# Performance work log

Measured on AMD Instinct MI355X. Metric: run time of the kernel, lower is better.

The kernel has to match this reference:

```python
import jax, jax.numpy as jnp
import numpy as np

EMBED_DIM = 384
MAX_LEN = 5000
TIMESTEP = 10000.0


def _build_table():
    pos = np.arange(MAX_LEN, dtype=np.float32)[:, None]
    div = np.exp(np.arange(0, EMBED_DIM, 2, dtype=np.float32) * (-np.log(TIMESTEP) / EMBED_DIM))
    pe = np.zeros((MAX_LEN, EMBED_DIM), dtype=np.float32)
    pe[:, 0::2] = np.sin(pos * div)
    pe[:, 1::2] = np.cos(pos * div)
    return jnp.asarray(pe)


def setup_inputs() -> dict:
    key = jax.random.key(0)
    x = jax.random.randint(key, (32, 512), 0, 16, dtype=jnp.int32)  # per-token durations
    pos_enc = _build_table()  # (MAX_LEN, EMBED_DIM) learned-free sinusoidal table
    return {"x": x, "pos_enc": pos_enc}


def reference(x, pos_enc):
    # x: (B, N) int durations; output: (B, T, D), T = max row-total frames
    cs = jnp.cumsum(x, axis=1)                 # (B, N) cumulative frame counts
    total = cs[:, -1]                          # (B,) frames per row
    T = int(np.asarray(jnp.max(cs)))           # concrete max total frames (data-dep, eval eagerly)
    starts = cs - x                            # (B, N) start frame of each token
    t = jnp.arange(T, dtype=cs.dtype)          # (T,) frame indices
    # token owning each frame: first index with cs > t
    tok = jax.vmap(lambda c: jnp.searchsorted(c, t, side='right'))(cs)  # (B, T)
    tok = jnp.minimum(tok, x.shape[1] - 1)     # clamp for padded frames
    pos = t[None, :] - jnp.take_along_axis(starts, tok, axis=1)         # (B, T) within-token position
    valid = t[None, :] < total[:, None]        # (B, T)
    pos = jnp.where(valid, pos, 0)
    emb = pos_enc[pos]                         # (B, T, D) gather
    return emb * valid[..., None].astype(emb.dtype)
```

## Files before the change

### kernel.cpp

```cpp
#include <hip/hip_runtime.h>
#include <hip/hip_bf16.h>


#define B 32
#define L 512
#define D 384
#define D4 (D / 4)

__global__ __launch_bounds__(64) void pe_cumsum_kernel(
    const int* __restrict__ x, int* __restrict__ cs) {
  const int b = blockIdx.x;
  const int lane = threadIdx.x;
  const int base = b * L + lane * 8;

  const int4* xr = reinterpret_cast<const int4*>(x + base);
  int4 a = xr[0];
  int4 c = xr[1];
  int v[8] = {a.x, a.y, a.z, a.w, c.x, c.y, c.z, c.w};

  int pref[8];
  int s = 0;
#pragma unroll
  for (int k = 0; k < 8; ++k) { s += v[k]; pref[k] = s; }

  int acc = s;
#pragma unroll
  for (int off = 1; off < 64; off <<= 1) {
    int n = __shfl_up(acc, off);
    if (lane >= off) acc += n;
  }
  const int offset = acc - s;

  int4 o0 = make_int4(offset + pref[0], offset + pref[1],
                      offset + pref[2], offset + pref[3]);
  int4 o1 = make_int4(offset + pref[4], offset + pref[5],
                      offset + pref[6], offset + pref[7]);
  int4* cr = reinterpret_cast<int4*>(cs + base);
  cr[0] = o0;
  cr[1] = o1;
}

__global__ __launch_bounds__(256) void pe_segcopy_kernel(
    const int* __restrict__ x, const int* __restrict__ cs,
    const float4* __restrict__ pe, float4* __restrict__ out, int T) {
  const int j = blockIdx.x;
  const int b = blockIdx.y;
  const int c = x[b * L + j];
  if (c == 0) return;
  const int start = cs[b * L + j] - c;

  float4* dst = out + ((size_t)b * T + start) * D4;
  const int n = c * D4;
  for (int i = threadIdx.x; i < n; i += 256) {
    dst[i] = pe[i];
  }
}

__global__ __launch_bounds__(256) void pe_tailzero_kernel(
    const int* __restrict__ cs, float4* __restrict__ out, int T) {
  const int b = blockIdx.y;
  const int total = cs[b * L + (L - 1)];
  const int n = (T - total) * D4;
  float4* dst = out + ((size_t)b * T + total) * D4;
  const float4 z = make_float4(0.f, 0.f, 0.f, 0.f);
  const int stride = gridDim.x * 256;
  for (int i = blockIdx.x * 256 + threadIdx.x; i < n; i += stride) {
    dst[i] = z;
  }
}

extern "C" void kernel_launch(void* const* d_in, const int* in_sizes, int n_in,
                              void* d_out, int out_size, void* d_ws, size_t ws_size,
                              hipStream_t stream) {
  const int* x = (const int*)d_in[0];
  const float* pe = (const float*)d_in[1];
  float* out = (float*)d_out;

  const int T = out_size / (B * D);

  int* cs = (int*)d_ws;

  pe_cumsum_kernel<<<B, 64, 0, stream>>>(x, cs);

  dim3 g2(L, B);
  pe_segcopy_kernel<<<g2, 256, 0, stream>>>(x, cs, (const float4*)pe,
                                            (float4*)out, T);

  dim3 g3(32, B);
  pe_tailzero_kernel<<<g3, 256, 0, stream>>>(cs, (float4*)out, T);
}
```

Measured before the change: 202.1 us.

## Build per-frame source-row map, then write output in one flat streaming kernel

The plan kernel now writes, for each output frame, the within-token position (or -1 for padding) into a workspace array. One grid-stride kernel then fills the whole output: each element looks up its row's source and copies a pe vector or writes zero, using nontemporal stores. This replaces the per-token segment-copy blocks, many of them tiny or empty, and the separate tail-zero kernel with one evenly balanced launch. The cost is that the plan kernel fills the map serially per lane, and the write kernel does an integer divide and an extra index load per element.

```diff
diff --git a/kernel.cpp b/kernel.cpp
--- a/kernel.cpp
+++ b/kernel.cpp
@@ -7,16 +7,18 @@
 #define D 384
 #define D4 (D / 4)
 
-__global__ __launch_bounds__(64) void pe_cumsum_kernel(
-    const int* __restrict__ x, int* __restrict__ cs) {
+typedef float f32x4 __attribute__((ext_vector_type(4)));
+
+__global__ __launch_bounds__(64) void pe_plan_kernel(
+    const int* __restrict__ x, int* __restrict__ rowsrc, int T) {
   const int b = blockIdx.x;
   const int lane = threadIdx.x;
   const int base = b * L + lane * 8;
 
   const int4* xr = reinterpret_cast<const int4*>(x + base);
   int4 a = xr[0];
-  int4 c = xr[1];
-  int v[8] = {a.x, a.y, a.z, a.w, c.x, c.y, c.z, c.w};
+  int4 c4 = xr[1];
+  int v[8] = {a.x, a.y, a.z, a.w, c4.x, c4.y, c4.z, c4.w};
 
   int pref[8];
   int s = 0;
@@ -29,43 +31,32 @@
     int n = __shfl_up(acc, off);
     if (lane >= off) acc += n;
   }
-  const int offset = acc - s;
+  const int lane_off = acc - s;
+  const int total = __shfl(acc, 63);
 
-  int4 o0 = make_int4(offset + pref[0], offset + pref[1],
-                      offset + pref[2], offset + pref[3]);
-  int4 o1 = make_int4(offset + pref[4], offset + pref[5],
-                      offset + pref[6], offset + pref[7]);
-  int4* cr = reinterpret_cast<int4*>(cs + base);
-  cr[0] = o0;
-  cr[1] = o1;
+  int* rs = rowsrc + (size_t)b * T;
+
+#pragma unroll
+  for (int k = 0; k < 8; ++k) {
+    const int c = v[k];
+    const int st = lane_off + pref[k] - c;
+    for (int p = 0; p < c; ++p) rs[st + p] = p;
+  }
+
+  for (int t = total + lane; t < T; t += 64) rs[t] = -1;
 }
 
-__global__ __launch_bounds__(256) void pe_segcopy_kernel(
-    const int* __restrict__ x, const int* __restrict__ cs,
-    const float4* __restrict__ pe, float4* __restrict__ out, int T) {
-  const int j = blockIdx.x;
-  const int b = blockIdx.y;
-  const int c = x[b * L + j];
-  if (c == 0) return;
-  const int start = cs[b * L + j] - c;
-
-  float4* dst = out + ((size_t)b * T + start) * D4;
-  const int n = c * D4;
-  for (int i = threadIdx.x; i < n; i += 256) {
-    dst[i] = pe[i];
-  }
-}
-
-__global__ __launch_bounds__(256) void pe_tailzero_kernel(
-    const int* __restrict__ cs, float4* __restrict__ out, int T) {
-  const int b = blockIdx.y;
-  const int total = cs[b * L + (L - 1)];
-  const int n = (T - total) * D4;
-  float4* dst = out + ((size_t)b * T + total) * D4;
-  const float4 z = make_float4(0.f, 0.f, 0.f, 0.f);
+__global__ __launch_bounds__(256) void pe_write_kernel(
+    const f32x4* __restrict__ pe, const int* __restrict__ rowsrc,
+    f32x4* __restrict__ out, int n4) {
   const int stride = gridDim.x * 256;
-  for (int i = blockIdx.x * 256 + threadIdx.x; i < n; i += stride) {
-    dst[i] = z;
+  for (int i = blockIdx.x * 256 + threadIdx.x; i < n4; i += stride) {
+    const int row = i / D4;
+    const int col = i - row * D4;
+    const int p = rowsrc[row];
+    f32x4 v = {0.f, 0.f, 0.f, 0.f};
+    if (p >= 0) v = pe[p * D4 + col];
+    __builtin_nontemporal_store(v, &out[i]);
   }
 }
 
@@ -78,14 +69,13 @@
 
   const int T = out_size / (B * D);
 
-  int* cs = (int*)d_ws;
+  int* rowsrc = (int*)d_ws;
 
-  pe_cumsum_kernel<<<B, 64, 0, stream>>>(x, cs);
+  pe_plan_kernel<<<B, 64, 0, stream>>>(x, rowsrc, T);
 
-  dim3 g2(L, B);
-  pe_segcopy_kernel<<<g2, 256, 0, stream>>>(x, cs, (const float4*)pe,
-                                            (float4*)out, T);
-
-  dim3 g3(32, B);
-  pe_tailzero_kernel<<<g3, 256, 0, stream>>>(cs, (float4*)out, T);
+  const int n4 = out_size / 4;
+  int blocks = (n4 + 255) / 256;
+  if (blocks > 2048) blocks = 2048;
+  pe_write_kernel<<<blocks, 256, 0, stream>>>(
+      (const f32x4*)pe, rowsrc, (f32x4*)out, n4);
 }
```

New measurement: 206.4 us. +2.2%, slower.
